# Performance work log

Measured on AMD Instinct MI355X. Metric: run time of the kernel, lower is better.

## Reference

```python
import jax, jax.numpy as jnp
import numpy as np

NUM_HEADS = 16
D_MODEL = 1024
DK = D_MODEL // NUM_HEADS


def setup_inputs() -> dict:
    key = jax.random.key(0)
    kH, kq, kk, kv, ko = jax.random.split(key, 5)
    scale = 0.02
    return {
        "H": jax.random.normal(kH, (4, 2048, D_MODEL), dtype=jnp.float32),
        "Wq": jax.random.normal(kq, (D_MODEL, D_MODEL), dtype=jnp.float32) * scale,
        "Wk": jax.random.normal(kk, (D_MODEL, D_MODEL), dtype=jnp.float32) * scale,
        "Wv": jax.random.normal(kv, (D_MODEL, D_MODEL), dtype=jnp.float32) * scale,
        "Wo": jax.random.normal(ko, (D_MODEL, D_MODEL), dtype=jnp.float32) * scale,
    }


def reference(H, Wq, Wk, Wv, Wo):
    b, T, d = H.shape
    n, dk = NUM_HEADS, DK
    # projections -> [b, n, T, dk]
    def split_heads(x):
        return x.reshape(b, T, n, dk).transpose(0, 2, 1, 3)
    Q = split_heads(H @ Wq)
    K = split_heads(H @ Wk)
    V = split_heads(H @ Wv)
    scores = jnp.einsum("bntd,bnsd->bnts", Q, K) / jnp.sqrt(jnp.float32(dk))
    causal = jnp.tril(jnp.ones((T, T), dtype=bool))
    scores = jnp.where(causal[None, None], scores, -jnp.inf)
    attn = jax.nn.softmax(scores, axis=-1)  # dropout rate 0 -> identity
    out = jnp.einsum("bnts,bnsd->bntd", attn, V)  # [b, n, T, dk]
    out = out.transpose(0, 2, 1, 3).reshape(b, T, n * dk)
    return out @ Wo
```

## Files before the change

kernel.cpp:

```cpp
#include <hip/hip_runtime.h>
#include <hip/hip_bf16.h>

#define T_SEQ 2048
#define DM 1024
#define DM2 2048
#define NH 16
#define DKH 64
#define NBATCH 4
#define MROWS (NBATCH*T_SEQ)

typedef __attribute__((ext_vector_type(8))) short bf16x8;
typedef __attribute__((ext_vector_type(4))) short bf16x4;
typedef __attribute__((ext_vector_type(4))) float f32x4;
typedef __attribute__((ext_vector_type(16))) float f32x16;
typedef __attribute__((ext_vector_type(4))) unsigned short u16x4;

#define NEG_INF (-__builtin_inff())

#if __has_builtin(__builtin_amdgcn_exp2f)
#define EXP2(x) __builtin_amdgcn_exp2f(x)
#else
#define EXP2(x) exp2f(x)
#endif

#define MFMA32(A,B,C) __builtin_amdgcn_mfma_f32_32x32x16_bf16(A,B,C,0,0,0)

static __device__ __forceinline__ unsigned short f2bf(float f){
  union { float f; unsigned u; } v; v.f = f;
  unsigned r = v.u + 0x7fffu + ((v.u >> 16) & 1u);
  return (unsigned short)(r >> 16);
}

static __device__ __forceinline__ unsigned short f2bfc(float f){
  union { __hip_bfloat16 h; unsigned short u; } cv;
  cv.h = __float2bfloat16(f);
  return cv.u;
}

static __device__ __forceinline__ void gload_lds16(const void* g, void* l){
  __builtin_amdgcn_global_load_lds(
      (const __attribute__((address_space(1))) void*)g,
      (__attribute__((address_space(3))) void*)l, 16, 0, 0);
}

__global__ __launch_bounds__(256) void convprep(
    const float* __restrict__ H,
    const float* __restrict__ W0, const float* __restrict__ W1,
    const float* __restrict__ W2, const float* __restrict__ W3,
    u16x4* __restrict__ Hb4,
    unsigned short* __restrict__ O0, unsigned short* __restrict__ O1,
    unsigned short* __restrict__ O2, unsigned short* __restrict__ O3)
{
  __shared__ float t[32][33];
  const int bid = blockIdx.x, tid = threadIdx.x;
  if (bid < 4096){
    const int z = bid >> 10, rem = bid & 1023;
    const int nx = (rem & 31)*32, kx = (rem >> 5)*32;
    const float* W = (z==0)?W0:(z==1)?W1:(z==2)?W2:W3;
    unsigned short* O = (z==0)?O0:(z==1)?O1:(z==2)?O2:O3;
    const float sc = (z==0) ? 0.18033688f : 1.0f;
    const int tx = tid & 31, ty = tid >> 5;
    #pragma unroll
    for (int i = 0; i < 4; ++i)
      t[ty + i*8][tx] = W[(size_t)(kx + ty + i*8)*DM + nx + tx];
    __syncthreads();
    #pragma unroll
    for (int i = 0; i < 4; ++i)
      O[(size_t)(nx + ty + i*8)*DM + kx + tx] = f2bf(t[tx][ty + i*8] * sc);
  } else {
    const int n4 = MROWS*DM/4;
    for (int i = (bid - 4096)*256 + tid; i < n4; i += 2048*256){
      float4 v = ((const float4*)H)[i];
      u16x4 o;
      o[0] = f2bf(v.x); o[1] = f2bf(v.y); o[2] = f2bf(v.z); o[3] = f2bf(v.w);
      Hb4[i] = o;
    }
  }
}

__global__ __launch_bounds__(512, 2) void gemm_qk8(
    const unsigned short* __restrict__ A, const unsigned short* __restrict__ Bt,
    unsigned short* __restrict__ C)
{
  __shared__ __attribute__((aligned(16))) unsigned short lds[2][32768];
  const int tid = threadIdx.x;
  const int w = tid >> 6, l = tid & 63;
  const int g = l >> 4, lr = l & 15;
  const int wr = w >> 2, wc = w & 3;
  const int bid = blockIdx.x;
  const int m0 = (bid & 31) * 256, n0 = (bid >> 5) * 256;

  const int c0 = (w*2)*64 + l, c1 = (w*2+1)*64 + l;
  const int r0 = c0 >> 3, gc0 = (c0 & 7) ^ (r0 & 7);
  const int r1 = c1 >> 3, gc1 = (c1 & 7) ^ (r1 & 7);

  auto STA = [&](int h, int t, int buf){
    gload_lds16(A + (size_t)(m0 + h*128 + r0)*DM + t*64 + gc0*8,
                (char*)lds + buf*65536 + h*16384 + c0*16);
    gload_lds16(A + (size_t)(m0 + h*128 + r1)*DM + t*64 + gc1*8,
                (char*)lds + buf*65536 + h*16384 + c1*16);
  };
  auto STB = [&](int h, int t, int buf){
    gload_lds16(Bt + (size_t)(n0 + h*128 + r0)*DM + t*64 + gc0*8,
                (char*)lds + buf*65536 + 32768 + h*16384 + c0*16);
    gload_lds16(Bt + (size_t)(n0 + h*128 + r1)*DM + t*64 + gc1*8,
                (char*)lds + buf*65536 + 32768 + h*16384 + c1*16);
  };

  f32x4 acc[8][4] = {};
  bf16x8 af[8], bf[8];

  STB(0,0,0); STB(1,0,0); STA(0,0,0); STA(1,0,0);
  STB(0,1,1); STB(1,1,1); STA(0,1,1); STA(1,1,1);
  asm volatile("s_waitcnt vmcnt(8)");
  __builtin_amdgcn_s_barrier();

#define RDA(BUF, MH) do{ _Pragma("unroll") for (int mi=0;mi<4;++mi){            \
    const int ra = ((MH)*4+mi)*16 + lr;                                         \
    _Pragma("unroll") for (int kc=0;kc<2;++kc)                                  \
      af[mi*2+kc] = *(const bf16x8*)((const char*)lds + (BUF)*65536             \
        + wr*16384 + ra*128 + ((kc*64+g*16) ^ ((ra&7)<<4))); } }while(0)
#define RDB(BUF, NHI) do{ _Pragma("unroll") for (int ni=0;ni<2;++ni){           \
    const int nt = (NHI)*2+ni; const int rb = (wc&1)*64 + nt*16 + lr;           \
    _Pragma("unroll") for (int kc=0;kc<2;++kc)                                  \
      bf[nt*2+kc] = *(const bf16x8*)((const char*)lds + (BUF)*65536 + 32768     \
        + (wc>>1)*16384 + rb*128 + ((kc*64+g*16) ^ ((rb&7)<<4))); } }while(0)
#define MF(MH, NHI) do{ _Pragma("unroll") for (int mi=0;mi<4;++mi)              \
    _Pragma("unroll") for (int ni=0;ni<2;++ni)                                  \
    _Pragma("unroll") for (int kc=0;kc<2;++kc)                                  \
      acc[(MH)*4+mi][(NHI)*2+ni] = __builtin_amdgcn_mfma_f32_16x16x32_bf16(     \
        af[mi*2+kc], bf[((NHI)*2+ni)*2+kc], acc[(MH)*4+mi][(NHI)*2+ni],0,0,0); }while(0)
#define WAITL0 do{ asm volatile("s_waitcnt lgkmcnt(0)");                        \
    __builtin_amdgcn_sched_barrier(0); }while(0)

  #pragma unroll 1
  for (int i = 0; i < 8; ++i){
    const int t1 = 2*i+1, t2 = 2*i+2, t3 = 2*i+3;
    RDA(0,0); RDB(0,0);
    if (i > 0) STA(0, t1, 1);
    asm volatile("s_waitcnt lgkmcnt(8)");
    __builtin_amdgcn_s_barrier();
    WAITL0;
    __builtin_amdgcn_s_setprio(1); MF(0,0); __builtin_amdgcn_s_setprio(0);
    __builtin_amdgcn_s_barrier();
    RDB(0,1);
    if (i > 0) STA(1, t1, 1);
    __builtin_amdgcn_s_barrier();
    WAITL0;
    __builtin_amdgcn_s_setprio(1); MF(0,1); __builtin_amdgcn_s_setprio(0);
    __builtin_amdgcn_s_barrier();
    RDA(0,1);
    if (i < 7) STB(0, t2, 0);
    __builtin_amdgcn_s_barrier();
    WAITL0;
    __builtin_amdgcn_s_setprio(1); MF(1,1); __builtin_amdgcn_s_setprio(0);
    __builtin_amdgcn_s_barrier();
    if (i < 7) STB(1, t2, 0);
    __builtin_amdgcn_s_setprio(1); MF(1,0); __builtin_amdgcn_s_setprio(0);
    if (i < 7) asm volatile("s_waitcnt vmcnt(4)");
    else       asm volatile("s_waitcnt vmcnt(0)");
    __builtin_amdgcn_s_barrier();
    RDA(1,0); RDB(1,0);
    if (i < 7) STA(0, t2, 0);
    asm volatile("s_waitcnt lgkmcnt(8)");
    __builtin_amdgcn_s_barrier();
    WAITL0;
    __builtin_amdgcn_s_setprio(1); MF(0,0); __builtin_amdgcn_s_setprio(0);
    __builtin_amdgcn_s_barrier();
    RDB(1,1);
    if (i < 7) STA(1, t2, 0);
    __builtin_amdgcn_s_barrier();
    WAITL0;
    __builtin_amdgcn_s_setprio(1); MF(0,1); __builtin_amdgcn_s_setprio(0);
    __builtin_amdgcn_s_barrier();
    RDA(1,1);
    if (i < 7) STB(0, t3, 1);
    __builtin_amdgcn_s_barrier();
    WAITL0;
    __builtin_amdgcn_s_setprio(1); MF(1,1); __builtin_amdgcn_s_setprio(0);
    __builtin_amdgcn_s_barrier();
    if (i < 7) STB(1, t3, 1);
    __builtin_amdgcn_s_setprio(1); MF(1,0); __builtin_amdgcn_s_setprio(0);
    asm volatile("s_waitcnt vmcnt(4)");
    __builtin_amdgcn_s_barrier();
  }
#undef RDA
#undef RDB
#undef MF
#undef WAITL0

  #pragma unroll
  for (int mt = 0; mt < 8; ++mt){
    const int row_b = m0 + wr*128 + mt*16 + 4*g;
    #pragma unroll
    for (int nt = 0; nt < 4; ++nt){
      const int col = n0 + wc*64 + nt*16 + lr;
      #pragma unroll
      for (int r = 0; r < 4; ++r)
        C[(size_t)(row_b + r)*DM2 + col] = f2bf(acc[mt][nt][r]);
    }
  }
}

template<bool F32OUT>
static __device__ __forceinline__ void gemm_body(
    const unsigned short* __restrict__ A, const unsigned short* __restrict__ Bt,
    void* __restrict__ Cp, int N, int K, int m0, int n0,
    unsigned short* a_lds, unsigned short* b_lds)
{
  const int tid = threadIdx.x;
  const int w = tid >> 6, l = tid & 63;
  const int g = l >> 4, lr = l & 15;
  const int wr = w >> 1, wc = w & 1;
  f32x4 acc[4][4] = {};
  const int nk = K >> 6;
  for (int ks = 0; ks < nk; ++ks){
    __syncthreads();
    const int k0 = ks << 6;
    #pragma unroll
    for (int i = 0; i < 4; ++i){
      int c = (w*4 + i)*64 + l;
      int row = c >> 3;
      int gc = (c & 7) ^ (row & 7);
      gload_lds16(A + (size_t)(m0 + row)*K + (k0 + gc*8), &a_lds[c*8]);
    }
    #pragma unroll
    for (int i = 0; i < 4; ++i){
      int c = (w*4 + i)*64 + l;
      int row = c >> 3;
      int gc = (c & 7) ^ (row & 7);
      gload_lds16(Bt + (size_t)(n0 + row)*K + (k0 + gc*8), &b_lds[c*8]);
    }
    __syncthreads();
    #pragma unroll
    for (int kc = 0; kc < 2; ++kc){
      bf16x8 af[4], bf_[4];
      #pragma unroll
      for (int mt = 0; mt < 4; ++mt){
        int row = wr*64 + mt*16 + lr;
        int off = row*128 + ((kc*64 + g*16) ^ ((row & 7) << 4));
        af[mt] = *(const bf16x8*)((const char*)a_lds + off);
      }
      #pragma unroll
      for (int nt = 0; nt < 4; ++nt){
        int row = wc*64 + nt*16 + lr;
        int off = row*128 + ((kc*64 + g*16) ^ ((row & 7) << 4));
        bf_[nt] = *(const bf16x8*)((const char*)b_lds + off);
      }
      #pragma unroll
      for (int mt = 0; mt < 4; ++mt)
        #pragma unroll
        for (int nt = 0; nt < 4; ++nt)
          acc[mt][nt] = __builtin_amdgcn_mfma_f32_16x16x32_bf16(af[mt], bf_[nt], acc[mt][nt], 0, 0, 0);
    }
  }
  #pragma unroll
  for (int mt = 0; mt < 4; ++mt){
    #pragma unroll
    for (int nt = 0; nt < 4; ++nt){
      const int col = n0 + wc*64 + nt*16 + lr;
      #pragma unroll
      for (int r = 0; r < 4; ++r){
        const int row = m0 + wr*64 + mt*16 + 4*g + r;
        if (F32OUT) ((float*)Cp)[(size_t)row*N + col] = acc[mt][nt][r];
        else ((unsigned short*)Cp)[(size_t)row*N + col] = f2bf(acc[mt][nt][r]);
      }
    }
  }
}

__global__ __launch_bounds__(256) void gemm_vt(
    const unsigned short* __restrict__ Wvt, const unsigned short* __restrict__ Hb,
    unsigned short* __restrict__ Vtb)
{
  __shared__ __attribute__((aligned(16))) unsigned short a_lds[128*64];
  __shared__ __attribute__((aligned(16))) unsigned short b_lds[128*64];
  gemm_body<false>(Wvt, Hb, Vtb, MROWS, DM, blockIdx.x*128, blockIdx.y*128, a_lds, b_lds);
}

__global__ __launch_bounds__(256) void gemm_out(
    const unsigned short* __restrict__ Ab, const unsigned short* __restrict__ Wot,
    float* __restrict__ Out)
{
  __shared__ __attribute__((aligned(16))) unsigned short a_lds[128*64];
  __shared__ __attribute__((aligned(16))) unsigned short b_lds[128*64];
  gemm_body<true>(Ab, Wot, Out, DM, DM, blockIdx.x*128, blockIdx.y*128, a_lds, b_lds);
}

static __device__ __forceinline__ void half_softmax(
    f32x16& st0, f32x16& st1, float& m_run, float& l_run,
    f32x16& acc0, f32x16& acc1, bf16x8 (&pb)[4],
    int kvb, int qg, bool fullT)
{
  if (!fullT){
    #pragma unroll
    for (int r = 0; r < 16; ++r){
      const int kvo = (r & 3) + 4*((r >> 2) & 1) + 16*(r >> 3);
      st0[r] = (kvb + kvo      <= qg) ? st0[r] : NEG_INF;
      st1[r] = (kvb + 32 + kvo <= qg) ? st1[r] : NEG_INF;
    }
  }
  float m01[8];
  #pragma unroll
  for (int r = 0; r < 8; ++r)
    m01[r] = fmaxf(fmaxf(st0[2*r], st0[2*r+1]), fmaxf(st1[2*r], st1[2*r+1]));
  float tm = fmaxf(fmaxf(fmaxf(m01[0],m01[1]), fmaxf(m01[2],m01[3])),
                   fmaxf(fmaxf(m01[4],m01[5]), fmaxf(m01[6],m01[7])));
  float mm = m_run;
  if (!__all(tm - m_run <= 8.f)){
    float tg = fmaxf(tm, __shfl_xor(tm, 32));
    const float mn = fmaxf(m_run, tg);
    const float fac = EXP2(m_run - mn);
    l_run *= fac;
    #pragma unroll
    for (int r = 0; r < 16; ++r){ acc0[r] *= fac; acc1[r] *= fac; }
    m_run = mn; mm = mn;
  }
  float ps0 = 0.f, ps1 = 0.f, ps2 = 0.f, ps3 = 0.f;
  #pragma unroll
  for (int r = 0; r < 4; ++r){
    float e0 = EXP2(st0[4*r+0]-mm), e1 = EXP2(st0[4*r+1]-mm);
    float e2 = EXP2(st0[4*r+2]-mm), e3 = EXP2(st0[4*r+3]-mm);
    float f0 = EXP2(st1[4*r+0]-mm), f1 = EXP2(st1[4*r+1]-mm);
    float f2 = EXP2(st1[4*r+2]-mm), f3 = EXP2(st1[4*r+3]-mm);
    ps0 += e0 + f0; ps1 += e1 + f1; ps2 += e2 + f2; ps3 += e3 + f3;
    st0[4*r+0]=e0; st0[4*r+1]=e1; st0[4*r+2]=e2; st0[4*r+3]=e3;
    st1[4*r+0]=f0; st1[4*r+1]=f1; st1[4*r+2]=f2; st1[4*r+3]=f3;
  }
  l_run += (ps0 + ps1) + (ps2 + ps3);
  #pragma unroll
  for (int m = 0; m < 2; ++m){
    bf16x8 t0, t1;
    #pragma unroll
    for (int i = 0; i < 8; ++i){
      t0[i] = (short)f2bfc(st0[8*m+i]);
      t1[i] = (short)f2bfc(st1[8*m+i]);
    }
    pb[m] = t0; pb[2+m] = t1;
  }
}

__global__ __launch_bounds__(512, 2) void attn_kernel(const unsigned short* __restrict__ QK,
                                                      const unsigned short* __restrict__ Vt,
                                                      unsigned short* __restrict__ Og)
{
  __shared__ __attribute__((aligned(16))) unsigned short k_lds[2][128*64];
  __shared__ __attribute__((aligned(16))) unsigned short v_lds[2][64*128];
  const int tid = threadIdx.x;
  const int w = tid >> 6, l = tid & 63;
  const int h1 = l >> 5, lq = l & 31;
  const int L = blockIdx.x;
  const int xcd = L & 7, idx = L >> 3;
  const int bh = xcd*8 + (idx & 7);
  const int pair = idx >> 3;
  const int b = bh >> 4, h = bh & 15;
  const size_t baseK = (size_t)(b*T_SEQ)*DM2 + 1024 + h*DKH;
  const size_t baseV = (size_t)(h*DKH)*MROWS + (size_t)b*T_SEQ;

  const int cA = tid, cB = tid + 512;
  const int krA = cA >> 3, krB = cB >> 3;
  const int kiA = (cA & 7) ^ (krA & 7), kiB = (cB & 7) ^ (krB & 7);
  const int kvA = 32*(krA >> 5) + 16*((krA >> 4) & 1) + 8*((krA >> 2) & 1) + 4*((krA >> 3) & 1) + (krA & 3);
  const int kvB = 32*(krB >> 5) + 16*((krB >> 4) & 1) + 8*((krB >> 2) & 1) + 4*((krB >> 3) & 1) + (krB & 3);
  const int vrA = cA >> 4, vgA = (cA & 15) ^ (vrA & 15);
  const int vrB = cB >> 4, vgB = (cB & 15) ^ (vrB & 15);

  auto STAGE = [&](int jt, int buf){
    const int j0s = jt * 128;
    gload_lds16(QK + baseK + (size_t)(j0s + kvA)*DM2 + kiA*8, &k_lds[buf][cA*8]);
    gload_lds16(QK + baseK + (size_t)(j0s + kvB)*DM2 + kiB*8, &k_lds[buf][cB*8]);
    gload_lds16(Vt + baseV + (size_t)vrA*MROWS + j0s + vgA*8, &v_lds[buf][cA*8]);
    gload_lds16(Vt + baseV + (size_t)vrB*MROWS + j0s + vgB*8, &v_lds[buf][cB*8]);
  };

#define ROUND(JT, CUR) do{                                                        \
    const int jt_ = (JT);                                                         \
    if (jt_ + 1 < ntiles) STAGE(jt_ + 1, (CUR)^1);                                \
    const int j0_ = jt_ * 128;                                                    \
    _Pragma("unroll")                                                             \
    for (int h2 = 0; h2 < 2; ++h2){                                               \
      if (j0_ + 64*h2 <= qhi){                                                    \
        f32x16 st0 = {}, st1 = {};                                                \
        __builtin_amdgcn_s_setprio(1);                                            \
        _Pragma("unroll")                                                         \
        for (int s = 0; s < 4; ++s){                                              \
          const int r0_ = 64*h2 + lq, r1_ = r0_ + 32;                             \
          bf16x8 kf0 = *(const bf16x8*)((const char*)k_lds[CUR] + r0_*128 + (((2*s + h1) ^ (r0_ & 7)) << 4)); \
          bf16x8 kf1 = *(const bf16x8*)((const char*)k_lds[CUR] + r1_*128 + (((2*s + h1) ^ (r1_ & 7)) << 4)); \
          st0 = MFMA32(kf0, qf[s], st0);                                          \
          st1 = MFMA32(kf1, qf[s], st1);                                          \
        }                                                                         \
        __builtin_amdgcn_s_setprio(0);                                            \
        bf16x8 pb[4];                                                             \
        half_softmax(st0, st1, m_run, l_run, acc0, acc1, pb,                      \
                     j0_ + 64*h2 + 8*h1, qg, (j0_ + 64*h2 + 63) <= qlo);          \
        __builtin_amdgcn_s_setprio(1);                                            \
        _Pragma("unroll")                                                         \
        for (int jl = 0; jl < 4; ++jl){                                           \
          const int vr0 = lq, vr1 = 32 + lq;                                      \
          bf16x8 vf0 = *(const bf16x8*)((const char*)v_lds[CUR] + vr0*256 + (((2*(4*h2 + jl) + h1) ^ (vr0 & 15)) << 4)); \
          bf16x8 vf1 = *(const bf16x8*)((const char*)v_lds[CUR] + vr1*256 + (((2*(4*h2 + jl) + h1) ^ (vr1 & 15)) << 4)); \
          acc0 = MFMA32(vf0, pb[jl], acc0);                                       \
          acc1 = MFMA32(vf1, pb[jl], acc1);                                       \
        }                                                                         \
        __builtin_amdgcn_s_setprio(0);                                            \
      }                                                                           \
    }                                                                             \
    __syncthreads();                                                              \
  } while(0)

  #pragma unroll 1
  for (int seg = 0; seg < 2; ++seg){
    const int qblk = seg ? pair : (7 - pair);
    const int q0 = qblk * 256;
    const int qlo = q0 + 32*w;
    const int qhi = qlo + 31;
    const int qg = qlo + lq;
    const size_t rowQ = (size_t)(b*T_SEQ + qg)*DM2 + h*DKH;
    bf16x8 qf[4];
    #pragma unroll
    for (int s = 0; s < 4; ++s)
      qf[s] = *(const bf16x8*)(QK + rowQ + 16*s + 8*h1);
    float m_run = NEG_INF, l_run = 0.f;
    f32x16 acc0 = {}, acc1 = {};
    const int ntiles = 2*qblk + 2;

    STAGE(0, 0);
    __syncthreads();

    #pragma unroll 1
    for (int jt = 0; jt < ntiles; jt += 2){
      ROUND(jt, 0);
      ROUND(jt + 1, 1);
    }

    const float ls = l_run + __shfl_xor(l_run, 32);
    const float inv = 1.f / ls;
    const size_t rowO = (size_t)(b*T_SEQ + qg)*DM + h*DKH;
    #pragma unroll
    for (int d = 0; d < 2; ++d){
      const f32x16& Aq = d ? acc1 : acc0;
      #pragma unroll
      for (int bb = 0; bb < 4; ++bb){
        unsigned u0 = (unsigned)f2bfc(Aq[4*bb+0]*inv) | ((unsigned)f2bfc(Aq[4*bb+1]*inv) << 16);
        unsigned u1 = (unsigned)f2bfc(Aq[4*bb+2]*inv) | ((unsigned)f2bfc(Aq[4*bb+3]*inv) << 16);
        uint2 uv; uv.x = u0; uv.y = u1;
        *(uint2*)(Og + rowO + 32*d + 8*bb + 4*h1) = uv;
      }
    }
  }
#undef ROUND
}

extern "C" void kernel_launch(void* const* d_in, const int* in_sizes, int n_in,
                              void* d_out, int out_size, void* d_ws, size_t ws_size,
                              hipStream_t stream)
{
  (void)in_sizes; (void)n_in; (void)out_size; (void)ws_size;
  const float* H  = (const float*)d_in[0];
  const float* Wq = (const float*)d_in[1];
  const float* Wk = (const float*)d_in[2];
  const float* Wv = (const float*)d_in[3];
  const float* Wo = (const float*)d_in[4];
  char* ws = (char*)d_ws;
  unsigned short* Hb   = (unsigned short*)(ws);
  unsigned short* Wqkt = (unsigned short*)(ws + 16777216);
  unsigned short* Wkt  = (unsigned short*)(ws + 18874368);
  unsigned short* Wvt  = (unsigned short*)(ws + 20971520);
  unsigned short* Wot  = (unsigned short*)(ws + 23068672);
  unsigned short* QKb  = (unsigned short*)(ws + 25165824);
  unsigned short* Vtb  = (unsigned short*)(ws + 58720256);
  unsigned short* Ab   = (unsigned short*)(ws + 75497472);

  convprep<<<6144, 256, 0, stream>>>(H, Wq, Wk, Wv, Wo,
                                     (u16x4*)Hb, Wqkt, Wkt, Wvt, Wot);
  gemm_qk8<<<256, 512, 0, stream>>>(Hb, Wqkt, QKb);
  gemm_vt<<<dim3(8,64), 256, 0, stream>>>(Wvt, Hb, Vtb);
  attn_kernel<<<dim3(256), 512, 0, stream>>>(QKb, Vtb, Ab);
  gemm_out<<<dim3(64,8), 256, 0, stream>>>(Ab, Wot, (float*)d_out);
}
```

Baseline: 152.5 us.

## Give each attention wave two query sub-tiles to reuse K/V LDS fragments

The attention kernel drops from 512 to 256 threads per block, and each wave now handles 64 query rows as two 32-row sub-tiles (A and B) instead of 32 rows. Each K and V fragment read from LDS feeds twice as many MFMAs, cutting LDS read traffic per FLOP. Each thread now issues four global-to-LDS loads per stage instead of two. The cost is a doubled accumulator and softmax state per thread, which raises register pressure, and launch bounds of (256,1) that may lower occupancy and the latency hiding of the softmax phase.

```diff
diff --git a/kernel.cpp b/kernel.cpp
--- a/kernel.cpp
+++ b/kernel.cpp
@@ -340,7 +340,7 @@
   }
 }
 
-__global__ __launch_bounds__(512, 2) void attn_kernel(const unsigned short* __restrict__ QK,
+__global__ __launch_bounds__(256, 1) void attn_kernel(const unsigned short* __restrict__ QK,
                                                       const unsigned short* __restrict__ Vt,
                                                       unsigned short* __restrict__ Og)
 {
@@ -352,25 +352,31 @@
   const int L = blockIdx.x;
   const int xcd = L & 7, idx = L >> 3;
   const int bh = xcd*8 + (idx & 7);
-  const int pair = idx >> 3;
+  const int quad = idx >> 3;
   const int b = bh >> 4, h = bh & 15;
   const size_t baseK = (size_t)(b*T_SEQ)*DM2 + 1024 + h*DKH;
   const size_t baseV = (size_t)(h*DKH)*MROWS + (size_t)b*T_SEQ;
 
-  const int cA = tid, cB = tid + 512;
-  const int krA = cA >> 3, krB = cB >> 3;
-  const int kiA = (cA & 7) ^ (krA & 7), kiB = (cB & 7) ^ (krB & 7);
-  const int kvA = 32*(krA >> 5) + 16*((krA >> 4) & 1) + 8*((krA >> 2) & 1) + 4*((krA >> 3) & 1) + (krA & 3);
-  const int kvB = 32*(krB >> 5) + 16*((krB >> 4) & 1) + 8*((krB >> 2) & 1) + 4*((krB >> 3) & 1) + (krB & 3);
-  const int vrA = cA >> 4, vgA = (cA & 15) ^ (vrA & 15);
-  const int vrB = cB >> 4, vgB = (cB & 15) ^ (vrB & 15);
+  int kvp[4], kip[4], vrp[4], vgp[4];
+  #pragma unroll
+  for (int i = 0; i < 4; ++i){
+    const int c = tid + 256*i;
+    const int kr = c >> 3;
+    kip[i] = (c & 7) ^ (kr & 7);
+    kvp[i] = 32*(kr >> 5) + 16*((kr >> 4) & 1) + 8*((kr >> 2) & 1) + 4*((kr >> 3) & 1) + (kr & 3);
+    const int vr = c >> 4;
+    vrp[i] = vr;
+    vgp[i] = (c & 15) ^ (vr & 15);
+  }
 
   auto STAGE = [&](int jt, int buf){
     const int j0s = jt * 128;
-    gload_lds16(QK + baseK + (size_t)(j0s + kvA)*DM2 + kiA*8, &k_lds[buf][cA*8]);
-    gload_lds16(QK + baseK + (size_t)(j0s + kvB)*DM2 + kiB*8, &k_lds[buf][cB*8]);
-    gload_lds16(Vt + baseV + (size_t)vrA*MROWS + j0s + vgA*8, &v_lds[buf][cA*8]);
-    gload_lds16(Vt + baseV + (size_t)vrB*MROWS + j0s + vgB*8, &v_lds[buf][cB*8]);
+    #pragma unroll
+    for (int i = 0; i < 4; ++i){
+      const int c = tid + 256*i;
+      gload_lds16(QK + baseK + (size_t)(j0s + kvp[i])*DM2 + kip[i]*8, &k_lds[buf][c*8]);
+      gload_lds16(Vt + baseV + (size_t)vrp[i]*MROWS + j0s + vgp[i]*8, &v_lds[buf][c*8]);
+    }
   };
 
 #define ROUND(JT, CUR) do{                                                        \
@@ -379,29 +385,32 @@
     const int j0_ = jt_ * 128;                                                    \
     _Pragma("unroll")                                                             \
     for (int h2 = 0; h2 < 2; ++h2){                                               \
-      if (j0_ + 64*h2 <= qhi){                                                    \
-        f32x16 st0 = {}, st1 = {};                                                \
+      if (j0_ + 64*h2 <= qhiB){                                                   \
+        const bool doA = (j0_ + 64*h2 <= qhiA);                                   \
+        f32x16 sA0 = {}, sA1 = {}, sB0 = {}, sB1 = {};                            \
         __builtin_amdgcn_s_setprio(1);                                            \
         _Pragma("unroll")                                                         \
         for (int s = 0; s < 4; ++s){                                              \
           const int r0_ = 64*h2 + lq, r1_ = r0_ + 32;                             \
           bf16x8 kf0 = *(const bf16x8*)((const char*)k_lds[CUR] + r0_*128 + (((2*s + h1) ^ (r0_ & 7)) << 4)); \
           bf16x8 kf1 = *(const bf16x8*)((const char*)k_lds[CUR] + r1_*128 + (((2*s + h1) ^ (r1_ & 7)) << 4)); \
-          st0 = MFMA32(kf0, qf[s], st0);                                          \
-          st1 = MFMA32(kf1, qf[s], st1);                                          \
+          if (doA){ sA0 = MFMA32(kf0, qfA[s], sA0); sA1 = MFMA32(kf1, qfA[s], sA1); } \
+          sB0 = MFMA32(kf0, qfB[s], sB0); sB1 = MFMA32(kf1, qfB[s], sB1);         \
         }                                                                         \
         __builtin_amdgcn_s_setprio(0);                                            \
-        bf16x8 pb[4];                                                             \
-        half_softmax(st0, st1, m_run, l_run, acc0, acc1, pb,                      \
-                     j0_ + 64*h2 + 8*h1, qg, (j0_ + 64*h2 + 63) <= qlo);          \
+        bf16x8 pbA[4], pbB[4];                                                    \
+        if (doA) half_softmax(sA0, sA1, mA, lA, accA0, accA1, pbA,                \
+                              j0_ + 64*h2 + 8*h1, qA, (j0_ + 64*h2 + 63) <= qloA);\
+        half_softmax(sB0, sB1, mB, lB, accB0, accB1, pbB,                         \
+                     j0_ + 64*h2 + 8*h1, qB, (j0_ + 64*h2 + 63) <= qloB);         \
         __builtin_amdgcn_s_setprio(1);                                            \
         _Pragma("unroll")                                                         \
         for (int jl = 0; jl < 4; ++jl){                                           \
           const int vr0 = lq, vr1 = 32 + lq;                                      \
           bf16x8 vf0 = *(const bf16x8*)((const char*)v_lds[CUR] + vr0*256 + (((2*(4*h2 + jl) + h1) ^ (vr0 & 15)) << 4)); \
           bf16x8 vf1 = *(const bf16x8*)((const char*)v_lds[CUR] + vr1*256 + (((2*(4*h2 + jl) + h1) ^ (vr1 & 15)) << 4)); \
-          acc0 = MFMA32(vf0, pb[jl], acc0);                                       \
-          acc1 = MFMA32(vf1, pb[jl], acc1);                                       \
+          if (doA){ accA0 = MFMA32(vf0, pbA[jl], accA0); accA1 = MFMA32(vf1, pbA[jl], accA1); } \
+          accB0 = MFMA32(vf0, pbB[jl], accB0); accB1 = MFMA32(vf1, pbB[jl], accB1); \
         }                                                                         \
         __builtin_amdgcn_s_setprio(0);                                            \
       }                                                                           \
@@ -411,18 +420,20 @@
 
   #pragma unroll 1
   for (int seg = 0; seg < 2; ++seg){
-    const int qblk = seg ? pair : (7 - pair);
+    const int qblk = seg ? quad : (7 - quad);
     const int q0 = qblk * 256;
-    const int qlo = q0 + 32*w;
-    const int qhi = qlo + 31;
-    const int qg = qlo + lq;
-    const size_t rowQ = (size_t)(b*T_SEQ + qg)*DM2 + h*DKH;
-    bf16x8 qf[4];
-    #pragma unroll
-    for (int s = 0; s < 4; ++s)
-      qf[s] = *(const bf16x8*)(QK + rowQ + 16*s + 8*h1);
-    float m_run = NEG_INF, l_run = 0.f;
-    f32x16 acc0 = {}, acc1 = {};
+    const int qloA = q0 + 64*w,  qhiA = qloA + 31, qA = qloA + lq;
+    const int qloB = qloA + 32,  qhiB = qloA + 63, qB = qA + 32;
+    const size_t rowQA = (size_t)(b*T_SEQ + qA)*DM2 + h*DKH;
+    const size_t rowQB = (size_t)(b*T_SEQ + qB)*DM2 + h*DKH;
+    bf16x8 qfA[4], qfB[4];
+    #pragma unroll
+    for (int s = 0; s < 4; ++s){
+      qfA[s] = *(const bf16x8*)(QK + rowQA + 16*s + 8*h1);
+      qfB[s] = *(const bf16x8*)(QK + rowQB + 16*s + 8*h1);
+    }
+    float mA = NEG_INF, lA = 0.f, mB = NEG_INF, lB = 0.f;
+    f32x16 accA0 = {}, accA1 = {}, accB0 = {}, accB1 = {};
     const int ntiles = 2*qblk + 2;
 
     STAGE(0, 0);
@@ -434,18 +445,36 @@
       ROUND(jt + 1, 1);
     }
 
-    const float ls = l_run + __shfl_xor(l_run, 32);
-    const float inv = 1.f / ls;
-    const size_t rowO = (size_t)(b*T_SEQ + qg)*DM + h*DKH;
-    #pragma unroll
-    for (int d = 0; d < 2; ++d){
-      const f32x16& Aq = d ? acc1 : acc0;
-      #pragma unroll
-      for (int bb = 0; bb < 4; ++bb){
-        unsigned u0 = (unsigned)f2bfc(Aq[4*bb+0]*inv) | ((unsigned)f2bfc(Aq[4*bb+1]*inv) << 16);
-        unsigned u1 = (unsigned)f2bfc(Aq[4*bb+2]*inv) | ((unsigned)f2bfc(Aq[4*bb+3]*inv) << 16);
-        uint2 uv; uv.x = u0; uv.y = u1;
-        *(uint2*)(Og + rowO + 32*d + 8*bb + 4*h1) = uv;
+    {
+      const float ls = lA + __shfl_xor(lA, 32);
+      const float inv = 1.f / ls;
+      const size_t rowO = (size_t)(b*T_SEQ + qA)*DM + h*DKH;
+      #pragma unroll
+      for (int d = 0; d < 2; ++d){
+        const f32x16& Aq = d ? accA1 : accA0;
+        #pragma unroll
+        for (int bb = 0; bb < 4; ++bb){
+          unsigned u0 = (unsigned)f2bfc(Aq[4*bb+0]*inv) | ((unsigned)f2bfc(Aq[4*bb+1]*inv) << 16);
+          unsigned u1 = (unsigned)f2bfc(Aq[4*bb+2]*inv) | ((unsigned)f2bfc(Aq[4*bb+3]*inv) << 16);
+          uint2 uv; uv.x = u0; uv.y = u1;
+          *(uint2*)(Og + rowO + 32*d + 8*bb + 4*h1) = uv;
+        }
+      }
+    }
+    {
+      const float ls = lB + __shfl_xor(lB, 32);
+      const float inv = 1.f / ls;
+      const size_t rowO = (size_t)(b*T_SEQ + qB)*DM + h*DKH;
+      #pragma unroll
+      for (int d = 0; d < 2; ++d){
+        const f32x16& Aq = d ? accB1 : accB0;
+        #pragma unroll
+        for (int bb = 0; bb < 4; ++bb){
+          unsigned u0 = (unsigned)f2bfc(Aq[4*bb+0]*inv) | ((unsigned)f2bfc(Aq[4*bb+1]*inv) << 16);
+          unsigned u1 = (unsigned)f2bfc(Aq[4*bb+2]*inv) | ((unsigned)f2bfc(Aq[4*bb+3]*inv) << 16);
+          uint2 uv; uv.x = u0; uv.y = u1;
+          *(uint2*)(Og + rowO + 32*d + 8*bb + 4*h1) = uv;
+        }
       }
     }
   }
@@ -476,6 +505,6 @@
                                      (u16x4*)Hb, Wqkt, Wkt, Wvt, Wot);
   gemm_qk8<<<256, 512, 0, stream>>>(Hb, Wqkt, QKb);
   gemm_vt<<<dim3(8,64), 256, 0, stream>>>(Wvt, Hb, Vtb);
-  attn_kernel<<<dim3(256), 512, 0, stream>>>(QKb, Vtb, Ab);
+  attn_kernel<<<dim3(256), 256, 0, stream>>>(QKb, Vtb, Ab);
   gemm_out<<<dim3(64,8), 256, 0, stream>>>(Ab, Wot, (float*)d_out);
 }
```

Measured after the change: 174.0 us. 14.1% more time.

## Halve attention query tile to 128 rows with 256-thread blocks and 512 blocks

Applied to the files above, without the earlier changes.

The attention kernel now uses 4 waves per block covering 128 query rows instead of 8 waves covering 256, and launches 512 blocks. Each block still pairs a long and a short query tile for causal load balance, now over 16 tiles, and handles an odd tile count with a tail round. The aim is more blocks, finer load balancing and more resident workgroups per CU. The cost is that each K/V tile staged in LDS is reused by fewer query rows, and each thread issues twice as many staging loads.

```diff
diff --git a/kernel.cpp b/kernel.cpp
--- a/kernel.cpp
+++ b/kernel.cpp
@@ -340,7 +340,7 @@
   }
 }
 
-__global__ __launch_bounds__(512, 2) void attn_kernel(const unsigned short* __restrict__ QK,
+__global__ __launch_bounds__(256, 2) void attn_kernel(const unsigned short* __restrict__ QK,
                                                       const unsigned short* __restrict__ Vt,
                                                       unsigned short* __restrict__ Og)
 {
@@ -352,25 +352,31 @@
   const int L = blockIdx.x;
   const int xcd = L & 7, idx = L >> 3;
   const int bh = xcd*8 + (idx & 7);
-  const int pair = idx >> 3;
+  const int p = idx >> 3;
   const int b = bh >> 4, h = bh & 15;
   const size_t baseK = (size_t)(b*T_SEQ)*DM2 + 1024 + h*DKH;
   const size_t baseV = (size_t)(h*DKH)*MROWS + (size_t)b*T_SEQ;
 
-  const int cA = tid, cB = tid + 512;
-  const int krA = cA >> 3, krB = cB >> 3;
-  const int kiA = (cA & 7) ^ (krA & 7), kiB = (cB & 7) ^ (krB & 7);
-  const int kvA = 32*(krA >> 5) + 16*((krA >> 4) & 1) + 8*((krA >> 2) & 1) + 4*((krA >> 3) & 1) + (krA & 3);
-  const int kvB = 32*(krB >> 5) + 16*((krB >> 4) & 1) + 8*((krB >> 2) & 1) + 4*((krB >> 3) & 1) + (krB & 3);
-  const int vrA = cA >> 4, vgA = (cA & 15) ^ (vrA & 15);
-  const int vrB = cB >> 4, vgB = (cB & 15) ^ (vrB & 15);
+  int kvp[4], kip[4], vrp[4], vgp[4];
+  #pragma unroll
+  for (int i = 0; i < 4; ++i){
+    const int c = tid + 256*i;
+    const int kr = c >> 3;
+    kip[i] = (c & 7) ^ (kr & 7);
+    kvp[i] = 32*(kr >> 5) + 16*((kr >> 4) & 1) + 8*((kr >> 2) & 1) + 4*((kr >> 3) & 1) + (kr & 3);
+    const int vr = c >> 4;
+    vrp[i] = vr;
+    vgp[i] = (c & 15) ^ (vr & 15);
+  }
 
   auto STAGE = [&](int jt, int buf){
     const int j0s = jt * 128;
-    gload_lds16(QK + baseK + (size_t)(j0s + kvA)*DM2 + kiA*8, &k_lds[buf][cA*8]);
-    gload_lds16(QK + baseK + (size_t)(j0s + kvB)*DM2 + kiB*8, &k_lds[buf][cB*8]);
-    gload_lds16(Vt + baseV + (size_t)vrA*MROWS + j0s + vgA*8, &v_lds[buf][cA*8]);
-    gload_lds16(Vt + baseV + (size_t)vrB*MROWS + j0s + vgB*8, &v_lds[buf][cB*8]);
+    #pragma unroll
+    for (int i = 0; i < 4; ++i){
+      const int c = tid + 256*i;
+      gload_lds16(QK + baseK + (size_t)(j0s + kvp[i])*DM2 + kip[i]*8, &k_lds[buf][c*8]);
+      gload_lds16(Vt + baseV + (size_t)vrp[i]*MROWS + j0s + vgp[i]*8, &v_lds[buf][c*8]);
+    }
   };
 
 #define ROUND(JT, CUR) do{                                                        \
@@ -411,8 +417,8 @@
 
   #pragma unroll 1
   for (int seg = 0; seg < 2; ++seg){
-    const int qblk = seg ? pair : (7 - pair);
-    const int q0 = qblk * 256;
+    const int qt = seg ? p : (15 - p);
+    const int q0 = qt * 128;
     const int qlo = q0 + 32*w;
     const int qhi = qlo + 31;
     const int qg = qlo + lq;
@@ -423,16 +429,18 @@
       qf[s] = *(const bf16x8*)(QK + rowQ + 16*s + 8*h1);
     float m_run = NEG_INF, l_run = 0.f;
     f32x16 acc0 = {}, acc1 = {};
-    const int ntiles = 2*qblk + 2;
+    const int ntiles = qt + 1;
 
     STAGE(0, 0);
     __syncthreads();
 
+    int jt = 0;
     #pragma unroll 1
-    for (int jt = 0; jt < ntiles; jt += 2){
+    for (; jt + 2 <= ntiles; jt += 2){
       ROUND(jt, 0);
       ROUND(jt + 1, 1);
     }
+    if (jt < ntiles) ROUND(jt, 0);
 
     const float ls = l_run + __shfl_xor(l_run, 32);
     const float inv = 1.f / ls;
@@ -476,6 +484,6 @@
                                      (u16x4*)Hb, Wqkt, Wkt, Wvt, Wot);
   gemm_qk8<<<256, 512, 0, stream>>>(Hb, Wqkt, QKb);
   gemm_vt<<<dim3(8,64), 256, 0, stream>>>(Wvt, Hb, Vtb);
-  attn_kernel<<<dim3(256), 512, 0, stream>>>(QKb, Vtb, Ab);
+  attn_kernel<<<dim3(512), 256, 0, stream>>>(QKb, Vtb, Ab);
   gemm_out<<<dim3(64,8), 256, 0, stream>>>(Ab, Wot, (float*)d_out);
 }
```

New measurement: 154.3 us. About the same (+1.2%).
